# Kernel tuning notes

Measured on AMD Instinct MI355X. Metric: run time of the kernel, lower is better.

Reference implementation:

```python
import jax, jax.numpy as jnp
import numpy as np
from math import factorial, sqrt

LMAX = 2
NB = 32
NRBF = 20
CUTOFF = 5.0
N_ATOMS = 20000
N_EDGES = 400000
T = 2
M = (LMAX + 1) ** 2
LIDX = np.repeat(np.arange(LMAX + 1), 2 * np.arange(LMAX + 1) + 1)  # l of each flat (l,m) index


def _cg_complex(j1, m1, j2, m2, j3, m3):
    # Racah formula for complex-SH Clebsch-Gordan coefficients
    if m3 != m1 + m2 or j3 < abs(j1 - j2) or j3 > j1 + j2:
        return 0.0
    f = factorial
    pref = sqrt((2 * j3 + 1) * f(j1 + j2 - j3) * f(j1 - j2 + j3) * f(-j1 + j2 + j3) / f(j1 + j2 + j3 + 1))
    pref *= sqrt(f(j1 + m1) * f(j1 - m1) * f(j2 + m2) * f(j2 - m2) * f(j3 + m3) * f(j3 - m3))
    kmin = max(0, j2 - j3 - m1, j1 + m2 - j3)
    kmax = min(j1 + j2 - j3, j1 - m1, j2 + m2)
    s = 0.0
    for k in range(kmin, kmax + 1):
        s += (-1) ** k / (f(k) * f(j1 + j2 - j3 - k) * f(j1 - m1 - k) * f(j2 + m2 - k) * f(j3 - j2 + m1 + k) * f(j3 - j1 - m2 + k))
    return pref * s


def _u_matrix(l):
    # real-SH = U @ complex-SH (rows: real m from -l..l, cols: complex m')
    U = np.zeros((2 * l + 1, 2 * l + 1), dtype=np.complex128)
    for m in range(-l, l + 1):
        if m == 0:
            U[l, l] = 1.0
        elif m > 0:
            U[l + m, l + m] = (-1) ** m / sqrt(2)
            U[l + m, l - m] = 1.0 / sqrt(2)
        else:
            mu = -m
            U[l + m, l + m] = 1j / sqrt(2)
            U[l + m, l - m] = -1j * (-1) ** mu / sqrt(2)
    return U


def _build_cg_rsh(lmax):
    # CG coefficients in the real-SH basis, parity invariant (odd l1+l2+l3 blocks zero)
    cg = np.zeros((M, M, M), dtype=np.float64)
    Us = [_u_matrix(l) for l in range(lmax + 1)]
    for l1 in range(lmax + 1):
        for l2 in range(lmax + 1):
            for l3 in range(lmax + 1):
                if (l1 + l2 + l3) % 2 == 1 or l3 < abs(l1 - l2) or l3 > l1 + l2:
                    continue
                Cc = np.zeros((2 * l1 + 1, 2 * l2 + 1, 2 * l3 + 1), dtype=np.complex128)
                for i, m1 in enumerate(range(-l1, l1 + 1)):
                    for j, m2 in enumerate(range(-l2, l2 + 1)):
                        m3 = m1 + m2
                        if abs(m3) <= l3:
                            Cc[i, j, l3 + m3] = _cg_complex(l1, m1, l2, m2, l3, m3)
                R = np.einsum('ai,bj,ck,ijk->abc', Us[l1], Us[l2], np.conj(Us[l3]), Cc)
                cg[l1 * l1:(l1 + 1) ** 2, l2 * l2:(l2 + 1) ** 2, l3 * l3:(l3 + 1) ** 2] = np.real(R)
    return cg.astype(np.float32)


CG = jnp.asarray(_build_cg_rsh(LMAX))   # [9, 9, 9]
LIDX_J = jnp.asarray(LIDX)


def _rsh(dirs):
    # real spherical harmonics up to l=2 on unit vectors, flat (l,m) order -> [P, 9]
    x, y, z = dirs[:, 0], dirs[:, 1], dirs[:, 2]
    c1 = 0.4886025119029199
    c2 = 1.0925484305920792
    return jnp.stack([
        jnp.full_like(x, 0.28209479177387814),
        c1 * y, c1 * z, c1 * x,
        c2 * x * y, c2 * y * z,
        0.31539156525252005 * (3.0 * z * z - 1.0),
        c2 * x * z,
        0.5462742152960396 * (x * x - y * y),
    ], axis=1)


def _forward(atomic_numbers, r_ij, idx_i, idx_j, emb, Wf, bf, Wm1, Wm2, Wm3, Wg, bg):
    d = jnp.linalg.norm(r_ij, axis=1)                      # [P]
    Y = _rsh(r_ij / d[:, None])                            # [P, 9]
    offsets = jnp.linspace(0.0, CUTOFF, NRBF)
    width = CUTOFF / (NRBF - 1)
    radial = jnp.exp(-0.5 / width ** 2 * (d[:, None] - offsets) ** 2)   # GaussianRBF [P, NRBF]
    fcut = jnp.where(d < CUTOFF, 0.5 * (jnp.cos(d * jnp.pi / CUTOFF) + 1.0), 0.0)  # CosineCutoff
    x0 = emb[atomic_numbers]                               # nuclear embedding [N, NB]
    x = jnp.concatenate([x0[:, None, :], jnp.zeros((x0.shape[0], M - 1, NB), x0.dtype)], axis=1)  # scalar2rsh
    for t in range(T):
        # SO3Convolution: per-edge radial filter per output degree l, cutoff gated
        Wl = ((radial @ Wf[t].T + bf[t]) * fcut[:, None]).reshape(-1, LMAX + 1, NB)
        xj = x[idx_j]                                      # gather neighbors [P, 9, NB]
        tbc = jnp.einsum('pa,abc->pbc', Y, CG)             # contract Y_ij with CG
        yij = jnp.einsum('pbc,pbn->pcn', tbc, xj) * Wl[:, LIDX_J, :]
        dx = jax.ops.segment_sum(yij, idx_i, num_segments=x.shape[0], indices_are_sorted=True)
        ddx = jnp.einsum('xcn,kn->xck', dx, Wm1[t])        # mixing1 (no bias)
        dx = dx + jnp.einsum('abc,xan,xbn->xcn', CG, dx, ddx)  # SO3TensorProduct
        dx = jnp.einsum('xcn,kn->xck', dx, Wm2[t])         # mixing2
        h = jax.nn.sigmoid((dx[:, 0, :] @ Wg[t].T + bg[t]).reshape(-1, LMAX + 1, NB))
        dx = dx * h[:, LIDX_J, :]                          # SO3ParametricGatedNonlinearity
        dx = jnp.einsum('xcn,kn->xck', dx, Wm3[t])         # mixing3
        x = x + dx
    return x                                               # multipole representation [N, 9, NB]


def setup_inputs():
    key = jax.random.key(0)
    ks = jax.random.split(key, 12)
    return {
        'atomic_numbers': jax.random.randint(ks[0], (N_ATOMS,), 1, 100),
        'r_ij': jax.random.normal(ks[1], (N_EDGES, 3), jnp.float32),
        'idx_i': jnp.sort(jax.random.randint(ks[2], (N_EDGES,), 0, N_ATOMS)),
        'idx_j': jax.random.randint(ks[3], (N_EDGES,), 0, N_ATOMS),
        'emb': jax.random.normal(ks[4], (101, NB), jnp.float32).at[0].set(0.0),
        'Wf': jax.random.normal(ks[5], (T, (LMAX + 1) * NB, NRBF), jnp.float32) / sqrt(NRBF),
        'bf': jnp.zeros((T, (LMAX + 1) * NB), jnp.float32),
        'Wm1': jax.random.normal(ks[6], (T, NB, NB), jnp.float32) / sqrt(NB),
        'Wm2': jax.random.normal(ks[7], (T, NB, NB), jnp.float32) / sqrt(NB),
        'Wm3': jax.random.normal(ks[8], (T, NB, NB), jnp.float32) / sqrt(NB),
        'Wg': jax.random.normal(ks[9], (T, (LMAX + 1) * NB, NB), jnp.float32) / sqrt(NB),
        'bg': jnp.zeros((T, (LMAX + 1) * NB), jnp.float32),
    }


def reference(atomic_numbers, r_ij, idx_i, idx_j, emb, Wf, bf, Wm1, Wm2, Wm3, Wg, bg):
    return _forward(atomic_numbers, r_ij, idx_i, idx_j, emb, Wf, bf, Wm1, Wm2, Wm3, Wg, bg)
```

## Files before the change

### kernel.cpp

```cpp
#include <hip/hip_runtime.h>

#define CHUNK 16

constexpr double CFACT[8] = {1.,1.,2.,6.,24.,120.,720.,5040.};

constexpr double csqrt(double x){
  if (x <= 0.0) return 0.0;
  double s = 1.0;
  while (x > 4.0)  { x *= 0.25; s *= 2.0; }
  while (x < 0.25) { x *= 4.0;  s *= 0.5; }
  double g = 1.0;
  for (int i=0;i<10;i++) g = 0.5*(g + x/g);
  return s*g;
}

constexpr double cg_complex(int j1,int m1,int j2,int m2,int j3,int m3){
  if (m3 != m1+m2 || j3 < (j1>j2?j1-j2:j2-j1) || j3 > j1+j2) return 0.0;
  double pref = csqrt((2.0*j3+1.0)*CFACT[j1+j2-j3]*CFACT[j1-j2+j3]*CFACT[-j1+j2+j3]/CFACT[j1+j2+j3+1]);
  pref *= csqrt(CFACT[j1+m1]*CFACT[j1-m1]*CFACT[j2+m2]*CFACT[j2-m2]*CFACT[j3+m3]*CFACT[j3-m3]);
  int kmin = 0;
  if (j2-j3-m1 > kmin) kmin = j2-j3-m1;
  if (j1+m2-j3 > kmin) kmin = j1+m2-j3;
  int kmax = j1+j2-j3;
  if (j1-m1 < kmax) kmax = j1-m1;
  if (j2+m2 < kmax) kmax = j2+m2;
  double s = 0.0;
  for (int k=kmin;k<=kmax;++k){
    double t = 1.0/(CFACT[k]*CFACT[j1+j2-j3-k]*CFACT[j1-m1-k]*CFACT[j2+m2-k]*CFACT[j3-j2+m1+k]*CFACT[j3-j1-m2+k]);
    s += (k&1)? -t : t;
  }
  return pref*s;
}

struct UR { int n; int mc[2]; double re[2]; double im[2]; };
constexpr UR u_row(int m){
  UR u{}; const double is2 = 0.70710678118654752440;
  if (m==0){ u.n=1; u.mc[0]=0; u.re[0]=1.0; u.im[0]=0.0; u.mc[1]=0; u.re[1]=0.0; u.im[1]=0.0; }
  else if (m>0){ u.n=2; u.mc[0]=m;  u.re[0]=((m&1)? -is2:is2); u.im[0]=0.0;
                        u.mc[1]=-m; u.re[1]=is2;               u.im[1]=0.0; }
  else { int mu=-m; u.n=2; u.mc[0]=m;  u.re[0]=0.0; u.im[0]=is2;
                           u.mc[1]=mu; u.re[1]=0.0; u.im[1]=((mu&1)? is2:-is2); }
  return u;
}

struct CGTab { float v[9][9][9]; };
constexpr CGTab build_cg(){
  CGTab g{};
  double cc[9][9][9] = {};
  for (int a=0;a<9;a++){
    int l1 = (a==0)?0:((a<4)?1:2); int m1 = a - (l1*l1+l1);
    for (int b=0;b<9;b++){
      int l2 = (b==0)?0:((b<4)?1:2); int m2 = b - (l2*l2+l2);
      int m3 = m1+m2;
      for (int l3=0;l3<=2;l3++){
        if (m3 < -l3 || m3 > l3) continue;
        cc[a][b][l3*l3+l3+m3] = cg_complex(l1,m1,l2,m2,l3,m3);
      }
    }
  }
  for (int l1=0;l1<=2;l1++) for (int l2=0;l2<=2;l2++) for (int l3=0;l3<=2;l3++){
    if (((l1+l2+l3)&1)==1) continue;
    int dl = (l1>l2)?(l1-l2):(l2-l1);
    if (l3 < dl || l3 > l1+l2) continue;
    for (int m1=-l1;m1<=l1;m1++) for (int m2=-l2;m2<=l2;m2++) for (int m3=-l3;m3<=l3;m3++){
      UR ua = u_row(m1), ub = u_row(m2), uc = u_row(m3);
      double acc = 0.0;
      for (int i=0;i<ua.n;i++) for (int j=0;j<ub.n;j++){
        double zr = ua.re[i]*ub.re[j] - ua.im[i]*ub.im[j];
        double zi = ua.re[i]*ub.im[j] + ua.im[i]*ub.re[j];
        for (int k=0;k<uc.n;k++){
          double rp = zr*uc.re[k] + zi*uc.im[k];
          if (rp != 0.0)
            acc += rp * cc[l1*l1+l1+ua.mc[i]][l2*l2+l2+ub.mc[j]][l3*l3+l3+uc.mc[k]];
        }
      }
      g.v[l1*l1+l1+m1][l2*l2+l2+m2][l3*l3+l3+m3] = (float)acc;
    }
  }
  return g;
}
constexpr CGTab CGT = build_cg();

__global__ void init_x_kernel(const int* __restrict__ Z, const float* __restrict__ emb,
                              float4* __restrict__ x4, float4* __restrict__ dx4, int n_atoms){
  int i = blockIdx.x*blockDim.x + threadIdx.x;
  if (i >= n_atoms*72) return;
  int atom = i/72, rem = i - atom*72;
  float4 v = make_float4(0.f,0.f,0.f,0.f);
  if (rem < 8) v = reinterpret_cast<const float4*>(emb)[Z[atom]*8 + rem];
  x4[i] = v;
  dx4[i] = make_float4(0.f,0.f,0.f,0.f);
}

template<bool FIRST>
__global__ __launch_bounds__(256) void edge_kernel(
    const float* __restrict__ r_ij, const int* __restrict__ idx_i, const int* __restrict__ idx_j,
    const float* __restrict__ x, const float* __restrict__ Wf_t, const float* __restrict__ bf_t,
    float* __restrict__ dx, int n_edges)
{
  int tid = threadIdx.x;
  int g = tid >> 5, lane = tid & 31;

  int base = (blockIdx.x*8 + g)*CHUNK;
  if (base >= n_edges) return;

  int pidx;
  {
    int e0 = base + (lane & 15);
    if (e0 > n_edges-1) e0 = n_edges-1;
    pidx = (lane < 16) ? idx_i[e0] : idx_j[e0];
  }
  float rv0, rv1;
  {
    long long rmax = (long long)n_edges*3 - 1;
    long long a0 = (long long)base*3 + lane;       if (a0 > rmax) a0 = rmax;
    long long a1 = (long long)base*3 + 32 + lane;  if (a1 > rmax) a1 = rmax;
    rv0 = r_ij[a0];
    rv1 = r_ij[a1];
  }

  float wfr[3][20]; float bfl[3];
  #pragma unroll
  for (int l=0;l<3;l++){
    const float* rp = Wf_t + (l*32+lane)*20;
    #pragma unroll
    for (int q=0;q<5;q++){
      float4 v4 = *reinterpret_cast<const float4*>(rp + q*4);
      wfr[l][q*4+0]=v4.x; wfr[l][q*4+1]=v4.y; wfr[l][q*4+2]=v4.z; wfr[l][q*4+3]=v4.w;
    }
    bfl[l] = bf_t[l*32+lane];
  }

  const float STEP  = 5.0f/19.0f;
  const float ALPHA = -0.5f/(STEP*STEP);
  float myoff = (float)lane * STEP;

  float racc[9];
  #pragma unroll
  for (int c=0;c<9;c++) racc[c]=0.f;
  int cur_i = -1;

  float xjn[9];
  float xjn0;
  {
    int j0 = __shfl(pidx, 16, 32);
    const float* xp = x + j0*288 + lane;
    if (FIRST){
      xjn0 = xp[0];
    } else {
      #pragma unroll
      for (int b=0;b<9;b++) xjn[b] = xp[b*32];
    }
  }

  #pragma unroll
  for (int k=0;k<CHUNK;k++){
    int e = base + k;
    if (e >= n_edges) break;

    float xj[9]; float xj0;
    if (FIRST){
      xj0 = xjn0;
    } else {
      #pragma unroll
      for (int b=0;b<9;b++) xj[b] = xjn[b];
    }

    if (k+1 < CHUNK){
      int jn = __shfl(pidx, 16+k+1, 32);
      const float* xp = x + jn*288 + lane;
      if (FIRST){
        xjn0 = xp[0];
      } else {
        #pragma unroll
        for (int b=0;b<9;b++) xjn[b] = xp[b*32];
      }
    }

    int ii = __shfl(pidx, k, 32);

    float rx = (3*k+0 < 32) ? __shfl(rv0, 3*k+0, 32) : __shfl(rv1, 3*k+0-32, 32);
    float ry = (3*k+1 < 32) ? __shfl(rv0, 3*k+1, 32) : __shfl(rv1, 3*k+1-32, 32);
    float rz = (3*k+2 < 32) ? __shfl(rv0, 3*k+2, 32) : __shfl(rv1, 3*k+2-32, 32);

    float d2 = fmaf(rx,rx,fmaf(ry,ry,rz*rz));
    float dd = sqrtf(d2);
    float inv = __fdividef(1.0f, dd);
    float X = rx*inv, Yv = ry*inv, Zv = rz*inv;
    const float c1 = 0.4886025119029199f, c2 = 1.0925484305920792f;
    float Y[9];
    Y[0]=0.28209479177387814f; Y[1]=c1*Yv; Y[2]=c1*Zv; Y[3]=c1*X;
    Y[4]=c2*X*Yv; Y[5]=c2*Yv*Zv; Y[6]=0.31539156525252005f*(3.f*Zv*Zv-1.f);
    Y[7]=c2*X*Zv; Y[8]=0.5462742152960396f*(X*X-Yv*Yv);

    float dtl = dd - myoff;
    float rbl = __expf(ALPHA*dtl*dtl);
    float wl0=bfl[0], wl1=bfl[1], wl2=bfl[2];
    #pragma unroll
    for (int r=0;r<20;r++){
      float rb = __shfl(rbl, r, 32);
      wl0 = fmaf(rb, wfr[0][r], wl0);
      wl1 = fmaf(rb, wfr[1][r], wl1);
      wl2 = fmaf(rb, wfr[2][r], wl2);
    }
    float fc = (dd < 5.0f) ? 0.5f*(__cosf(dd*0.6283185307179586f)+1.0f) : 0.0f;
    wl0*=fc; wl1*=fc; wl2*=fc;

    if (ii != cur_i){
      if (cur_i >= 0){
        float* dp = dx + cur_i*288 + lane;
        #pragma unroll
        for (int c=0;c<9;c++){ atomicAdd(dp + c*32, racc[c]); racc[c]=0.f; }
      }
      cur_i = ii;
    }

    if (FIRST){
      racc[0] = fmaf(wl0, Y[0]*xj0, racc[0]);
      #pragma unroll
      for (int c=1;c<4;c++) racc[c] = fmaf(wl1, Y[c]*xj0, racc[c]);
      #pragma unroll
      for (int c=4;c<9;c++) racc[c] = fmaf(wl2, Y[c]*xj0, racc[c]);
    } else {
      float yv[9];
      #pragma unroll
      for (int c=0;c<9;c++) yv[c]=0.f;
      #pragma unroll
      for (int a=0;a<9;a++){
        #pragma unroll
        for (int b=0;b<9;b++){
          bool any = false;
          #pragma unroll
          for (int c=0;c<9;c++) any = any | (CGT.v[a][b][c] != 0.f);
          if (any){
            float p = Y[a]*xj[b];
            #pragma unroll
            for (int c=0;c<9;c++){
              if (CGT.v[a][b][c] != 0.f) yv[c] = fmaf(CGT.v[a][b][c], p, yv[c]);
            }
          }
        }
      }
      racc[0] = fmaf(wl0, yv[0], racc[0]);
      #pragma unroll
      for (int c=1;c<4;c++) racc[c] = fmaf(wl1, yv[c], racc[c]);
      #pragma unroll
      for (int c=4;c<9;c++) racc[c] = fmaf(wl2, yv[c], racc[c]);
    }
  }
  if (cur_i >= 0){
    float* dp = dx + cur_i*288 + lane;
    #pragma unroll
    for (int c=0;c<9;c++) atomicAdd(dp + c*32, racc[c]);
  }
}

__global__ __launch_bounds__(256) void atom_kernel(
    float* __restrict__ x, float* __restrict__ dxg,
    const float* __restrict__ Wm1_t, const float* __restrict__ Wm2_t, const float* __restrict__ Wm3_t,
    const float* __restrict__ Wg_t, const float* __restrict__ bg_t, int n_atoms)
{
  __shared__ __align__(16) float tile[8][288];
  int tid = threadIdx.x;
  int g = tid>>5, k = tid&31;
  int atom = blockIdx.x*8 + g;
  if (atom >= n_atoms) return;
  float* tg = &tile[g][0];
  const float4* t4 = reinterpret_cast<const float4*>(tg);

  float* dp = dxg + atom*288 + k;
  float v[9];
  #pragma unroll
  for (int c=0;c<9;c++){ v[c]=dp[c*32]; tg[c*32+k]=v[c]; dp[c*32]=0.f; }

  float wr[32];
  {
    const float4* w4 = reinterpret_cast<const float4*>(Wm1_t + k*32);
    #pragma unroll
    for (int q=0;q<8;q++){ float4 a=w4[q]; wr[4*q]=a.x; wr[4*q+1]=a.y; wr[4*q+2]=a.z; wr[4*q+3]=a.w; }
  }
  float u[9];
  #pragma unroll
  for (int c=0;c<9;c++){
    float s=0.f;
    #pragma unroll
    for (int q=0;q<8;q++){
      float4 tv = t4[c*8+q];
      s = fmaf(tv.x, wr[4*q+0], s); s = fmaf(tv.y, wr[4*q+1], s);
      s = fmaf(tv.z, wr[4*q+2], s); s = fmaf(tv.w, wr[4*q+3], s);
    }
    u[c]=s;
  }

  float w[9];
  #pragma unroll
  for (int c=0;c<9;c++) w[c]=v[c];
  #pragma unroll
  for (int a=0;a<9;a++){
    #pragma unroll
    for (int b=0;b<9;b++){
      bool any = false;
      #pragma unroll
      for (int c=0;c<9;c++) any = any | (CGT.v[a][b][c] != 0.f);
      if (any){
        float p = v[a]*u[b];
        #pragma unroll
        for (int c=0;c<9;c++){
          if (CGT.v[a][b][c] != 0.f) w[c] = fmaf(CGT.v[a][b][c], p, w[c]);
        }
      }
    }
  }

  #pragma unroll
  for (int c=0;c<9;c++) tg[c*32+k]=w[c];
  {
    const float4* w4 = reinterpret_cast<const float4*>(Wm2_t + k*32);
    #pragma unroll
    for (int q=0;q<8;q++){ float4 a=w4[q]; wr[4*q]=a.x; wr[4*q+1]=a.y; wr[4*q+2]=a.z; wr[4*q+3]=a.w; }
  }
  float p[9];
  #pragma unroll
  for (int c=0;c<9;c++){
    float s=0.f;
    #pragma unroll
    for (int q=0;q<8;q++){
      float4 tv = t4[c*8+q];
      s = fmaf(tv.x, wr[4*q+0], s); s = fmaf(tv.y, wr[4*q+1], s);
      s = fmaf(tv.z, wr[4*q+2], s); s = fmaf(tv.w, wr[4*q+3], s);
    }
    p[c]=s;
  }

  tg[k] = p[0];
  float s0=bg_t[k], s1=bg_t[32+k], s2=bg_t[64+k];
  {
    const float4* wg0 = reinterpret_cast<const float4*>(Wg_t + (     k)*32);
    const float4* wg1 = reinterpret_cast<const float4*>(Wg_t + (32 + k)*32);
    const float4* wg2 = reinterpret_cast<const float4*>(Wg_t + (64 + k)*32);
    #pragma unroll
    for (int q=0;q<8;q++){
      float4 tv = t4[q];
      float4 a0 = wg0[q], a1 = wg1[q], a2 = wg2[q];
      s0 = fmaf(tv.x,a0.x,s0); s0 = fmaf(tv.y,a0.y,s0); s0 = fmaf(tv.z,a0.z,s0); s0 = fmaf(tv.w,a0.w,s0);
      s1 = fmaf(tv.x,a1.x,s1); s1 = fmaf(tv.y,a1.y,s1); s1 = fmaf(tv.z,a1.z,s1); s1 = fmaf(tv.w,a1.w,s1);
      s2 = fmaf(tv.x,a2.x,s2); s2 = fmaf(tv.y,a2.y,s2); s2 = fmaf(tv.z,a2.z,s2); s2 = fmaf(tv.w,a2.w,s2);
    }
  }
  float h0 = 1.f/(1.f+__expf(-s0));
  float h1 = 1.f/(1.f+__expf(-s1));
  float h2 = 1.f/(1.f+__expf(-s2));

  float q9[9];
  q9[0]=p[0]*h0;
  #pragma unroll
  for (int c=1;c<4;c++) q9[c]=p[c]*h1;
  #pragma unroll
  for (int c=4;c<9;c++) q9[c]=p[c]*h2;

  #pragma unroll
  for (int c=0;c<9;c++) tg[c*32+k]=q9[c];
  {
    const float4* w4 = reinterpret_cast<const float4*>(Wm3_t + k*32);
    #pragma unroll
    for (int q=0;q<8;q++){ float4 a=w4[q]; wr[4*q]=a.x; wr[4*q+1]=a.y; wr[4*q+2]=a.z; wr[4*q+3]=a.w; }
  }
  float* xo = x + atom*288 + k;
  #pragma unroll
  for (int c=0;c<9;c++){
    float s=0.f;
    #pragma unroll
    for (int q=0;q<8;q++){
      float4 tv = t4[c*8+q];
      s = fmaf(tv.x, wr[4*q+0], s); s = fmaf(tv.y, wr[4*q+1], s);
      s = fmaf(tv.z, wr[4*q+2], s); s = fmaf(tv.w, wr[4*q+3], s);
    }
    xo[c*32] += s;
  }
}

extern "C" void kernel_launch(void* const* d_in, const int* in_sizes, int n_in,
                              void* d_out, int out_size, void* d_ws, size_t ws_size,
                              hipStream_t stream)
{
  const int*   Z    = (const int*)d_in[0];
  const float* r_ij = (const float*)d_in[1];
  const int*   idxi = (const int*)d_in[2];
  const int*   idxj = (const int*)d_in[3];
  const float* emb  = (const float*)d_in[4];
  const float* Wf   = (const float*)d_in[5];
  const float* bf   = (const float*)d_in[6];
  const float* Wm1  = (const float*)d_in[7];
  const float* Wm2  = (const float*)d_in[8];
  const float* Wm3  = (const float*)d_in[9];
  const float* Wg   = (const float*)d_in[10];
  const float* bg   = (const float*)d_in[11];
  int n_atoms = in_sizes[0];
  int n_edges = in_sizes[1]/3;

  float* x  = (float*)d_out;
  float* dx = (float*)d_ws;

  init_x_kernel<<<(n_atoms*72+255)/256,256,0,stream>>>(Z, emb, (float4*)x, (float4*)dx, n_atoms);

  int eblocks = (n_edges + 8*CHUNK - 1)/(8*CHUNK);
  int ablocks = (n_atoms + 7)/8;

  edge_kernel<true><<<eblocks,256,0,stream>>>(r_ij, idxi, idxj, x, Wf, bf, dx, n_edges);
  atom_kernel<<<ablocks,256,0,stream>>>(x, dx, Wm1, Wm2, Wm3, Wg, bg, n_atoms);

  edge_kernel<false><<<eblocks,256,0,stream>>>(r_ij, idxi, idxj, x,
                                        Wf + 96*20, bf + 96, dx, n_edges);
  atom_kernel<<<ablocks,256,0,stream>>>(x, dx,
                                        Wm1 + 1024, Wm2 + 1024, Wm3 + 1024,
                                        Wg + 96*32, bg + 96, n_atoms);
}
```

Measured before the change: 413.6 us.

## Stage radial filter weights in LDS and stream edge data with software prefetch

```diff
diff --git a/kernel.cpp b/kernel.cpp
--- a/kernel.cpp
+++ b/kernel.cpp
@@ -98,38 +98,24 @@
     const float* __restrict__ x, const float* __restrict__ Wf_t, const float* __restrict__ bf_t,
     float* __restrict__ dx, int n_edges)
 {
+  __shared__ float WfL[3*20*32];
   int tid = threadIdx.x;
+  for (int i = tid; i < 1920; i += 256){
+    int l  = i / 640;
+    int rn = i - l*640;
+    int r  = rn >> 5;
+    int n  = rn & 31;
+    WfL[i] = Wf_t[(l*32 + n)*20 + r];
+  }
+  __syncthreads();
+
   int g = tid >> 5, lane = tid & 31;
-
   int base = (blockIdx.x*8 + g)*CHUNK;
   if (base >= n_edges) return;
-
-  int pidx;
-  {
-    int e0 = base + (lane & 15);
-    if (e0 > n_edges-1) e0 = n_edges-1;
-    pidx = (lane < 16) ? idx_i[e0] : idx_j[e0];
-  }
-  float rv0, rv1;
-  {
-    long long rmax = (long long)n_edges*3 - 1;
-    long long a0 = (long long)base*3 + lane;       if (a0 > rmax) a0 = rmax;
-    long long a1 = (long long)base*3 + 32 + lane;  if (a1 > rmax) a1 = rmax;
-    rv0 = r_ij[a0];
-    rv1 = r_ij[a1];
-  }
-
-  float wfr[3][20]; float bfl[3];
-  #pragma unroll
-  for (int l=0;l<3;l++){
-    const float* rp = Wf_t + (l*32+lane)*20;
-    #pragma unroll
-    for (int q=0;q<5;q++){
-      float4 v4 = *reinterpret_cast<const float4*>(rp + q*4);
-      wfr[l][q*4+0]=v4.x; wfr[l][q*4+1]=v4.y; wfr[l][q*4+2]=v4.z; wfr[l][q*4+3]=v4.w;
-    }
-    bfl[l] = bf_t[l*32+lane];
-  }
+  const int nend = n_edges;
+
+  float bfl0 = bf_t[lane], bfl1 = bf_t[32+lane], bfl2 = bf_t[64+lane];
+  const float* wfp = WfL + lane;
 
   const float STEP  = 5.0f/19.0f;
   const float ALPHA = -0.5f/(STEP*STEP);
@@ -140,48 +126,40 @@
   for (int c=0;c<9;c++) racc[c]=0.f;
   int cur_i = -1;
 
-  float xjn[9];
-  float xjn0;
+  int   ii_c = idx_i[base];
+  float rx = r_ij[3*base+0], ry = r_ij[3*base+1], rz = r_ij[3*base+2];
+  float xj[9]; float xj0;
   {
-    int j0 = __shfl(pidx, 16, 32);
+    int j0 = idx_j[base];
     const float* xp = x + j0*288 + lane;
-    if (FIRST){
-      xjn0 = xp[0];
-    } else {
-      #pragma unroll
-      for (int b=0;b<9;b++) xjn[b] = xp[b*32];
-    }
-  }
-
-  #pragma unroll
+    if (FIRST){ xj0 = xp[0]; }
+    else {
+      #pragma unroll
+      for (int b=0;b<9;b++) xj[b] = xp[b*32];
+    }
+  }
+  int e1 = (base+1 < nend) ? base+1 : nend-1;
+  int j_next = idx_j[e1];
+
+  #pragma unroll 2
   for (int k=0;k<CHUNK;k++){
     int e = base + k;
-    if (e >= n_edges) break;
-
-    float xj[9]; float xj0;
-    if (FIRST){
-      xj0 = xjn0;
-    } else {
-      #pragma unroll
-      for (int b=0;b<9;b++) xj[b] = xjn[b];
-    }
-
-    if (k+1 < CHUNK){
-      int jn = __shfl(pidx, 16+k+1, 32);
-      const float* xp = x + jn*288 + lane;
-      if (FIRST){
-        xjn0 = xp[0];
-      } else {
+    if (e >= nend) break;
+
+    int en = (e+1 < nend) ? e+1 : nend-1;
+    int   ii_n = idx_i[en];
+    float rxn = r_ij[3*en+0], ryn = r_ij[3*en+1], rzn = r_ij[3*en+2];
+    float xjn[9]; float xjn0;
+    {
+      const float* xp = x + j_next*288 + lane;
+      if (FIRST){ xjn0 = xp[0]; }
+      else {
         #pragma unroll
         for (int b=0;b<9;b++) xjn[b] = xp[b*32];
       }
     }
-
-    int ii = __shfl(pidx, k, 32);
-
-    float rx = (3*k+0 < 32) ? __shfl(rv0, 3*k+0, 32) : __shfl(rv1, 3*k+0-32, 32);
-    float ry = (3*k+1 < 32) ? __shfl(rv0, 3*k+1, 32) : __shfl(rv1, 3*k+1-32, 32);
-    float rz = (3*k+2 < 32) ? __shfl(rv0, 3*k+2, 32) : __shfl(rv1, 3*k+2-32, 32);
+    int en2 = (e+2 < nend) ? e+2 : nend-1;
+    int j_n2 = idx_j[en2];
 
     float d2 = fmaf(rx,rx,fmaf(ry,ry,rz*rz));
     float dd = sqrtf(d2);
@@ -195,24 +173,24 @@
 
     float dtl = dd - myoff;
     float rbl = __expf(ALPHA*dtl*dtl);
-    float wl0=bfl[0], wl1=bfl[1], wl2=bfl[2];
+    float wl0=bfl0, wl1=bfl1, wl2=bfl2;
     #pragma unroll
     for (int r=0;r<20;r++){
       float rb = __shfl(rbl, r, 32);
-      wl0 = fmaf(rb, wfr[0][r], wl0);
-      wl1 = fmaf(rb, wfr[1][r], wl1);
-      wl2 = fmaf(rb, wfr[2][r], wl2);
+      wl0 = fmaf(rb, wfp[(    r)*32], wl0);
+      wl1 = fmaf(rb, wfp[(20+ r)*32], wl1);
+      wl2 = fmaf(rb, wfp[(40+ r)*32], wl2);
     }
     float fc = (dd < 5.0f) ? 0.5f*(__cosf(dd*0.6283185307179586f)+1.0f) : 0.0f;
     wl0*=fc; wl1*=fc; wl2*=fc;
 
-    if (ii != cur_i){
+    if (ii_c != cur_i){
       if (cur_i >= 0){
         float* dp = dx + cur_i*288 + lane;
         #pragma unroll
         for (int c=0;c<9;c++){ atomicAdd(dp + c*32, racc[c]); racc[c]=0.f; }
       }
-      cur_i = ii;
+      cur_i = ii_c;
     }
 
     if (FIRST){
@@ -246,6 +224,13 @@
       for (int c=1;c<4;c++) racc[c] = fmaf(wl1, yv[c], racc[c]);
       #pragma unroll
       for (int c=4;c<9;c++) racc[c] = fmaf(wl2, yv[c], racc[c]);
+    }
+
+    ii_c = ii_n; rx = rxn; ry = ryn; rz = rzn; j_next = j_n2;
+    if (FIRST){ xj0 = xjn0; }
+    else {
+      #pragma unroll
+      for (int b=0;b<9;b++) xj[b] = xjn[b];
     }
   }
   if (cur_i >= 0){
```

New measurement: 444.5 us. 1.07x slower.
